# Kernel optimization log

Measured on AMD Instinct MI355X. Metric: run time of the kernel, lower is better.

Reference implementation:

```python
import jax, jax.numpy as jnp
import numpy as np

BATCH = 16384
NUM_CLASSES = 1024  # power of 2 -> exact complete binary NBDT hierarchy, depth 10


def setup_inputs() -> dict:
    key = jax.random.key(0)
    outputs = jax.random.normal(key, (BATCH, NUM_CLASSES), dtype=jnp.float32)
    return {"outputs": outputs}


def reference(outputs) -> jnp.ndarray:
    """SoftEmbeddedDecisionRules.forward over a complete balanced binary tree.

    For every internal node: node_logits[child] = mean of outputs over the
    leaf classes under that child (get_node_logits), probs = softmax over
    children (get_all_node_outputs), and class_probs[:, leaves_under_child]
    *= probs[:, child] (traverse_tree). With a balanced binary tree, nodes at
    depth d split classes into 2^d blocks of 2 equal halves, so each level
    vectorizes into one reshape/mean/softmax/multiply.
    """
    B, C = outputs.shape
    depth = int(np.log2(C))
    class_probs = jnp.ones((B, C), dtype=outputs.dtype)
    for d in range(depth):
        n_nodes = 1 << d            # nodes at this tree level
        blk = C // (2 * n_nodes)    # leaves per child
        # gather-mean: node logits [B, n_nodes, 2]
        node_logits = outputs.reshape(B, n_nodes, 2, blk).mean(axis=-1)
        probs = jax.nn.softmax(node_logits, axis=-1)  # per-node softmax over children
        # scatter-multiply into class probabilities
        class_probs = (class_probs.reshape(B, n_nodes, 2, blk)
                       * probs[..., None]).reshape(B, C)
    return class_probs
```

## Files before the change

kernel.cpp:

```cpp
#include <hip/hip_runtime.h>

#define NBDT_BATCH 16384
#define NBDT_C 1024

__device__ __forceinline__ float fast_sigmoid(float x) {
    return __builtin_amdgcn_rcpf(1.0f + __expf(-x));
}

__global__ __launch_bounds__(256) void nbdt_kernel(const float* __restrict__ x,
                                                   float* __restrict__ y) {
    const int gtid = blockIdx.x * 256 + threadIdx.x;
    const int row  = gtid >> 6;
    const int lane = threadIdx.x & 63;
    const size_t base = (size_t)row * NBDT_C + (size_t)lane * 16;

    const float4* xin = reinterpret_cast<const float4*>(x + base);
    float4 v0 = xin[0];
    float4 v1 = xin[1];
    float4 v2 = xin[2];
    float4 v3 = xin[3];
    float e[16] = {v0.x, v0.y, v0.z, v0.w,
                   v1.x, v1.y, v1.z, v1.w,
                   v2.x, v2.y, v2.z, v2.w,
                   v3.x, v3.y, v3.z, v3.w};

    float s2[8], s4[4], s8[2], s16;
#pragma unroll
    for (int i = 0; i < 8; ++i) s2[i] = e[2 * i] + e[2 * i + 1];
#pragma unroll
    for (int i = 0; i < 4; ++i) s4[i] = s2[2 * i] + s2[2 * i + 1];
#pragma unroll
    for (int i = 0; i < 2; ++i) s8[i] = s4[2 * i] + s4[2 * i + 1];
    s16 = s8[0] + s8[1];

    float t16 = __shfl_xor(s16, 1);
    float s32 = s16 + t16;
    float t32 = __shfl_xor(s32, 2);
    float s64 = s32 + t32;
    float t64 = __shfl_xor(s64, 4);
    float s128 = s64 + t64;
    float t128 = __shfl_xor(s128, 8);
    float s256 = s128 + t128;
    float t256 = __shfl_xor(s256, 16);
    float s512 = s256 + t256;
    float t512 = __shfl_xor(s512, 32);

    float P = fast_sigmoid((s512 - t512) * (1.0f / 512.0f));
    P *= fast_sigmoid((s256 - t256) * (1.0f / 256.0f));
    P *= fast_sigmoid((s128 - t128) * (1.0f / 128.0f));
    P *= fast_sigmoid((s64 - t64) * (1.0f / 64.0f));
    P *= fast_sigmoid((s32 - t32) * (1.0f / 32.0f));
    P *= fast_sigmoid((s16 - t16) * (1.0f / 16.0f));

    float c8[2];
    {
        float p = fast_sigmoid((s8[0] - s8[1]) * 0.125f);
        c8[0] = P * p;
        c8[1] = P - c8[0];
    }
    float c4[4];
#pragma unroll
    for (int h = 0; h < 2; ++h) {
        float p = fast_sigmoid((s4[2 * h] - s4[2 * h + 1]) * 0.25f);
        c4[2 * h] = c8[h] * p;
        c4[2 * h + 1] = c8[h] - c4[2 * h];
    }
    float c2[8];
#pragma unroll
    for (int q = 0; q < 4; ++q) {
        float p = fast_sigmoid((s2[2 * q] - s2[2 * q + 1]) * 0.5f);
        c2[2 * q] = c4[q] * p;
        c2[2 * q + 1] = c4[q] - c2[2 * q];
    }
    float o[16];
#pragma unroll
    for (int k = 0; k < 8; ++k) {
        float p = fast_sigmoid(e[2 * k] - e[2 * k + 1]);
        o[2 * k] = c2[k] * p;
        o[2 * k + 1] = c2[k] - o[2 * k];
    }

    float4* yout = reinterpret_cast<float4*>(y + base);
    yout[0] = make_float4(o[0], o[1], o[2], o[3]);
    yout[1] = make_float4(o[4], o[5], o[6], o[7]);
    yout[2] = make_float4(o[8], o[9], o[10], o[11]);
    yout[3] = make_float4(o[12], o[13], o[14], o[15]);
}

extern "C" void kernel_launch(void* const* d_in, const int* in_sizes, int n_in,
                              void* d_out, int out_size, void* d_ws, size_t ws_size,
                              hipStream_t stream) {
    const float* x = (const float*)d_in[0];
    float* y = (float*)d_out;
    dim3 grid(NBDT_BATCH / 4);
    dim3 block(256);
    nbdt_kernel<<<grid, block, 0, stream>>>(x, y);
}
```

Baseline: 117.7 us.

## Interleave row layout so each lane loads coalesced float4 chunks strided by 256

Changes the per-lane data assignment. Each lane now reads four float4 chunks spaced 256 floats apart instead of 16 contiguous floats, so every wave-wide load instruction touches one contiguous 1 KB span. The hierarchy reduction is reorganised to match: four independent butterfly shuffle chains, one per chunk, replace the single chain, and the top two tree levels are combined in registers. This adds more shuffles and sigmoid evaluations per lane in exchange for better-coalesced memory access on a bandwidth-bound kernel.

```diff
diff --git a/kernel.cpp b/kernel.cpp
--- a/kernel.cpp
+++ b/kernel.cpp
@@ -9,82 +9,64 @@
 
 __global__ __launch_bounds__(256) void nbdt_kernel(const float* __restrict__ x,
                                                    float* __restrict__ y) {
-    const int gtid = blockIdx.x * 256 + threadIdx.x;
-    const int row  = gtid >> 6;
+    const int wave = (blockIdx.x * 256 + threadIdx.x) >> 6;
     const int lane = threadIdx.x & 63;
-    const size_t base = (size_t)row * NBDT_C + (size_t)lane * 16;
+    const size_t rowbase = (size_t)wave * NBDT_C + (size_t)lane * 4;
 
-    const float4* xin = reinterpret_cast<const float4*>(x + base);
-    float4 v0 = xin[0];
-    float4 v1 = xin[1];
-    float4 v2 = xin[2];
-    float4 v3 = xin[3];
-    float e[16] = {v0.x, v0.y, v0.z, v0.w,
-                   v1.x, v1.y, v1.z, v1.w,
-                   v2.x, v2.y, v2.z, v2.w,
-                   v3.x, v3.y, v3.z, v3.w};
-
-    float s2[8], s4[4], s8[2], s16;
+    float e[4][4];
 #pragma unroll
-    for (int i = 0; i < 8; ++i) s2[i] = e[2 * i] + e[2 * i + 1];
-#pragma unroll
-    for (int i = 0; i < 4; ++i) s4[i] = s2[2 * i] + s2[2 * i + 1];
-#pragma unroll
-    for (int i = 0; i < 2; ++i) s8[i] = s4[2 * i] + s4[2 * i + 1];
-    s16 = s8[0] + s8[1];
-
-    float t16 = __shfl_xor(s16, 1);
-    float s32 = s16 + t16;
-    float t32 = __shfl_xor(s32, 2);
-    float s64 = s32 + t32;
-    float t64 = __shfl_xor(s64, 4);
-    float s128 = s64 + t64;
-    float t128 = __shfl_xor(s128, 8);
-    float s256 = s128 + t128;
-    float t256 = __shfl_xor(s256, 16);
-    float s512 = s256 + t256;
-    float t512 = __shfl_xor(s512, 32);
-
-    float P = fast_sigmoid((s512 - t512) * (1.0f / 512.0f));
-    P *= fast_sigmoid((s256 - t256) * (1.0f / 256.0f));
-    P *= fast_sigmoid((s128 - t128) * (1.0f / 128.0f));
-    P *= fast_sigmoid((s64 - t64) * (1.0f / 64.0f));
-    P *= fast_sigmoid((s32 - t32) * (1.0f / 32.0f));
-    P *= fast_sigmoid((s16 - t16) * (1.0f / 16.0f));
-
-    float c8[2];
-    {
-        float p = fast_sigmoid((s8[0] - s8[1]) * 0.125f);
-        c8[0] = P * p;
-        c8[1] = P - c8[0];
-    }
-    float c4[4];
-#pragma unroll
-    for (int h = 0; h < 2; ++h) {
-        float p = fast_sigmoid((s4[2 * h] - s4[2 * h + 1]) * 0.25f);
-        c4[2 * h] = c8[h] * p;
-        c4[2 * h + 1] = c8[h] - c4[2 * h];
-    }
-    float c2[8];
-#pragma unroll
-    for (int q = 0; q < 4; ++q) {
-        float p = fast_sigmoid((s2[2 * q] - s2[2 * q + 1]) * 0.5f);
-        c2[2 * q] = c4[q] * p;
-        c2[2 * q + 1] = c4[q] - c2[2 * q];
-    }
-    float o[16];
-#pragma unroll
-    for (int k = 0; k < 8; ++k) {
-        float p = fast_sigmoid(e[2 * k] - e[2 * k + 1]);
-        o[2 * k] = c2[k] * p;
-        o[2 * k + 1] = c2[k] - o[2 * k];
+    for (int k = 0; k < 4; ++k) {
+        float4 v = *reinterpret_cast<const float4*>(x + rowbase + k * 256);
+        e[k][0] = v.x; e[k][1] = v.y; e[k][2] = v.z; e[k][3] = v.w;
     }
 
-    float4* yout = reinterpret_cast<float4*>(y + base);
-    yout[0] = make_float4(o[0], o[1], o[2], o[3]);
-    yout[1] = make_float4(o[4], o[5], o[6], o[7]);
-    yout[2] = make_float4(o[8], o[9], o[10], o[11]);
-    yout[3] = make_float4(o[12], o[13], o[14], o[15]);
+    float s2[4][2], s4[4], s256[4];
+    float d4[4], d8[4], d16[4], d32[4], d64[4], d128[4];
+#pragma unroll
+    for (int k = 0; k < 4; ++k) {
+        s2[k][0] = e[k][0] + e[k][1];
+        s2[k][1] = e[k][2] + e[k][3];
+        s4[k] = s2[k][0] + s2[k][1];
+        float acc = s4[k];
+        float t;
+        t = __shfl_xor(acc, 1);  d4[k]   = acc - t;  acc += t;
+        t = __shfl_xor(acc, 2);  d8[k]   = acc - t;  acc += t;
+        t = __shfl_xor(acc, 4);  d16[k]  = acc - t;  acc += t;
+        t = __shfl_xor(acc, 8);  d32[k]  = acc - t;  acc += t;
+        t = __shfl_xor(acc, 16); d64[k]  = acc - t;  acc += t;
+        t = __shfl_xor(acc, 32); d128[k] = acc - t;  acc += t;
+        s256[k] = acc;
+    }
+
+    const float S512a = s256[0] + s256[1];
+    const float S512b = s256[2] + s256[3];
+    const float pTop = fast_sigmoid((S512a - S512b) * (1.0f / 512.0f));
+    const float qTop = 1.0f - pTop;
+    const float p01  = fast_sigmoid((s256[0] - s256[1]) * (1.0f / 256.0f));
+    const float p23  = fast_sigmoid((s256[2] - s256[3]) * (1.0f / 256.0f));
+    float P[4];
+    P[0] = pTop * p01;  P[1] = pTop - P[0];
+    P[2] = qTop * p23;  P[3] = qTop - P[2];
+
+#pragma unroll
+    for (int k = 0; k < 4; ++k) {
+        float Pk = P[k];
+        Pk *= fast_sigmoid(d128[k] * (1.0f / 128.0f));
+        Pk *= fast_sigmoid(d64[k]  * (1.0f / 64.0f));
+        Pk *= fast_sigmoid(d32[k]  * (1.0f / 32.0f));
+        Pk *= fast_sigmoid(d16[k]  * (1.0f / 16.0f));
+        Pk *= fast_sigmoid(d8[k]   * (1.0f / 8.0f));
+        Pk *= fast_sigmoid(d4[k]   * (1.0f / 4.0f));
+
+        float c0 = Pk * fast_sigmoid((s2[k][0] - s2[k][1]) * 0.5f);
+        float c1 = Pk - c0;
+        float4 o;
+        o.x = c0 * fast_sigmoid(e[k][0] - e[k][1]);
+        o.y = c0 - o.x;
+        o.z = c1 * fast_sigmoid(e[k][2] - e[k][3]);
+        o.w = c1 - o.z;
+        *reinterpret_cast<float4*>(y + rowbase + k * 256) = o;
+    }
 }
 
 extern "C" void kernel_launch(void* const* d_in, const int* in_sizes, int n_in,
```

After: 108.7 us. -7.6%, faster.
